# Optimization experiments

Measured on AMD Instinct MI355X. Metric: run time of the kernel, lower is better.

The kernel has to match this reference:

```python
import jax, jax.numpy as jnp
import numpy as np

RES = 32  # voxel grid resolution per axis (cfg.MODEL.NEURAL_POINTS.VOXEL_RES)


def upsample_ac(x, s):
    """Bilinear upsample with align_corners=True. x: [B,C,h,w] -> [B,C,h*s,w*s]."""
    if s == 1:
        return x
    B, C, h, w = x.shape
    H, W = h * s, w * s
    ys = jnp.arange(H, dtype=x.dtype) * ((h - 1) / (H - 1))
    xs = jnp.arange(W, dtype=x.dtype) * ((w - 1) / (W - 1))
    y0 = jnp.floor(ys).astype(jnp.int32)
    x0 = jnp.floor(xs).astype(jnp.int32)
    y1 = jnp.minimum(y0 + 1, h - 1)
    x1 = jnp.minimum(x0 + 1, w - 1)
    wy = (ys - y0.astype(x.dtype))[:, None]  # [H,1]
    wx = (xs - x0.astype(x.dtype))[None, :]  # [1,W]
    top = x[:, :, y0, :]
    bot = x[:, :, y1, :]
    a = top[..., x0]; b = top[..., x1]; c = bot[..., x0]; d = bot[..., x1]
    return (a * (1 - wx) + b * wx) * (1 - wy) + (c * (1 - wx) + d * wx) * wy


def vox_closest(pos):
    """construct_vox_points_closest: per occupied voxel, index of point closest to
    the voxel's point centroid. pos: [N,3] -> [RES^3] int32 indices."""
    N = pos.shape[0]
    Vn = RES ** 3
    mn = pos.min(0)
    mx = pos.max(0)
    vsz = (mx - mn) / RES  # obtain_voxel_size_based_grid_res
    coord = jnp.clip(jnp.floor((pos - mn) / vsz).astype(jnp.int32), 0, RES - 1)
    vid = (coord[:, 0] * RES + coord[:, 1]) * RES + coord[:, 2]  # [N]
    cnt = jax.ops.segment_sum(jnp.ones((N,), pos.dtype), vid, Vn)
    cen = jax.ops.segment_sum(pos, vid, Vn) / jnp.maximum(cnt, 1.0)[:, None]
    d = jnp.sum((pos - cen[vid]) ** 2, axis=-1)  # [N] dist^2 to own-voxel centroid
    dmin = jax.ops.segment_min(d, vid, Vn)
    cand = jnp.where(d <= dmin[vid], jnp.arange(N, dtype=jnp.int32), N)
    midx = jax.ops.segment_min(cand, vid, Vn)
    return jnp.where(midx >= N, 0, midx)  # guard (rare) empty voxels


def reference(rgb, f1, f2, f3, points_pos, points_dir, W1, b1, W2, b2, points_mask):
    V, _, H, W = rgb.shape
    N = V * H * W
    C = 59
    # valid_index = where(points_mask == 1) (mask is all ones -> identity gather)
    valid = jnp.nonzero(points_mask[0] == 1, size=N, fill_value=0)[0]
    pos = points_pos[0, valid]          # [N,3]
    pdir = points_dir[0, valid]         # [N,3]
    # project_point_feats: upsample each pyramid level to full res, concat channels
    ups = [upsample_ac(rgb, 1), upsample_ac(f1, 2), upsample_ac(f2, 4), upsample_ac(f3, 8)]
    pif = jnp.concatenate(ups, axis=1)                       # [V,59,H,W]
    pif = jnp.transpose(pif, (0, 2, 3, 1)).reshape(N, C)     # [N,59]
    color = jax.lax.stop_gradient(jnp.transpose(rgb, (0, 2, 3, 1)).reshape(N, 3))
    pif = pif[valid]
    color = color[valid]
    emb = jnp.concatenate([pif, pdir], axis=-1)              # [N,62]
    midx = vox_closest(pos)                                  # [32768]
    sel_emb = emb[midx]
    sel_pos = pos[midx]
    sel_color = color[midx]
    sel_dir = pdir[midx]
    # point_mlp (premlp_init): 62 -> 256 -> 256
    h = jax.nn.relu(sel_emb @ W1 + b1)
    points_embedding = h @ W2 + b2
    return points_embedding, sel_pos, sel_color, sel_dir


def setup_inputs() -> dict:
    key = jax.random.key(0)
    ks = jax.random.split(key, 10)
    V, H, W = 8, 240, 320
    N = V * H * W
    return {
        "rgb": jax.random.uniform(ks[0], (V, 3, H, W), jnp.float32),
        "f1": jax.random.normal(ks[1], (V, 8, H // 2, W // 2), jnp.float32),
        "f2": jax.random.normal(ks[2], (V, 16, H // 4, W // 4), jnp.float32),
        "f3": jax.random.normal(ks[3], (V, 32, H // 8, W // 8), jnp.float32),
        "points_pos": jax.random.uniform(ks[4], (1, N, 3), jnp.float32),
        "points_dir": jax.random.normal(ks[5], (1, N, 3), jnp.float32),
        "W1": jax.random.normal(ks[6], (62, 256), jnp.float32) * 0.05,
        "b1": jnp.zeros((256,), jnp.float32),
        "W2": jax.random.normal(ks[7], (256, 256), jnp.float32) * 0.05,
        "b2": jnp.zeros((256,), jnp.float32),
        "points_mask": jnp.ones((1, N), jnp.int32),
    }
```

## Files before the change

### kernel.cpp

```cpp
#include <hip/hip_runtime.h>
#include <hip/hip_bf16.h>
#include <limits.h>
#include <stddef.h>

#define NPTS   614400
#define RESV   32
#define NVOX   (RESV*RESV*RESV)
#define IMG_H  240
#define IMG_W  320
#define IMG_HW (IMG_H*IMG_W)
#define INF    __builtin_inff()
#define CAP    64
#define CAPP   32
#define SPILLCAP 4096
#define NBKT   128
#define BCAP   6144
#define BOVFCAP 4096

typedef __attribute__((ext_vector_type(8))) short short8;
typedef __attribute__((ext_vector_type(4))) short s16x4;
typedef __attribute__((ext_vector_type(4))) float f32x4;
typedef float f32x4u __attribute__((ext_vector_type(4), aligned(4)));

__device__ __forceinline__ float fadd_(float a, float b){
#pragma clang fp contract(off)
  return a + b;
}
__device__ __forceinline__ float fsub_(float a, float b){
#pragma clang fp contract(off)
  return a - b;
}
__device__ __forceinline__ float fmul_(float a, float b){
#pragma clang fp contract(off)
  return a * b;
}
__device__ __forceinline__ float fdiv_(float a, float b){
#pragma clang fp contract(off)
  return a / b;
}

__device__ __forceinline__ short f2bf(float x){
  __hip_bfloat16 h = __float2bfloat16(x);
  return *reinterpret_cast<short*>(&h);
}

__global__ void k_prep(int* __restrict__ cnt, int* __restrict__ spillcnt,
                       int* __restrict__ gbase,
                       const float* __restrict__ W1, const float* __restrict__ W2,
                       short* __restrict__ W1t, short* __restrict__ W2t,
                       const float* __restrict__ pos,
                       f32x4* __restrict__ pmin, f32x4* __restrict__ pmax,
                       const float* __restrict__ f1, const float* __restrict__ f2,
                       const float* __restrict__ f3,
                       float* __restrict__ f1t, float* __restrict__ f2t,
                       float* __restrict__ f3t, int tposed){
  int gid = blockIdx.x*blockDim.x + threadIdx.x;
  int stride = gridDim.x*blockDim.x;
  if (gid < NVOX) cnt[gid] = 0;
  if (gid == 0){ spillcnt[0] = 0; spillcnt[1] = 0; }
  if (gid < NBKT) gbase[gid] = 0;
  if (gid < 256*64){
    int n = gid >> 6, k = gid & 63;
    W1t[gid] = (k < 62) ? f2bf(W1[k*256 + n]) : (short)0;
  } else if (gid < 256*64 + 256*256){
    int j = gid - 256*64;
    int n = j >> 8, k = j & 255;
    W2t[j] = f2bf(W2[k*256 + n]);
  }

  if (tposed){
    for (int p = gid; p < 8*19200; p += stride){
      int img = p / 19200, pix = p - img*19200;
      const float* s = f1 + (size_t)img*8*19200 + pix;
      float r[8];
      #pragma unroll
      for (int c = 0; c < 8; c++) r[c] = s[(size_t)c*19200];
      float* d = f1t + (size_t)p*8;
      *(f32x4*)&d[0] = (f32x4){r[0],r[1],r[2],r[3]};
      *(f32x4*)&d[4] = (f32x4){r[4],r[5],r[6],r[7]};
    }
    for (int p = gid; p < 8*4800; p += stride){
      int img = p / 4800, pix = p - img*4800;
      const float* s = f2 + (size_t)img*16*4800 + pix;
      float* d = f2t + (size_t)p*16;
      #pragma unroll
      for (int cq = 0; cq < 4; cq++){
        f32x4 v = { s[(size_t)(4*cq+0)*4800], s[(size_t)(4*cq+1)*4800],
                    s[(size_t)(4*cq+2)*4800], s[(size_t)(4*cq+3)*4800] };
        *(f32x4*)&d[4*cq] = v;
      }
    }
    for (int p = gid; p < 8*1200; p += stride){
      int img = p / 1200, pix = p - img*1200;
      const float* s = f3 + (size_t)img*32*1200 + pix;
      float* d = f3t + (size_t)p*32;
      #pragma unroll
      for (int cq = 0; cq < 8; cq++){
        f32x4 v = { s[(size_t)(4*cq+0)*1200], s[(size_t)(4*cq+1)*1200],
                    s[(size_t)(4*cq+2)*1200], s[(size_t)(4*cq+3)*1200] };
        *(f32x4*)&d[4*cq] = v;
      }
    }
  }

  const f32x4* p4 = (const f32x4*)pos;
  float mn[3] = {  INF,  INF,  INF };
  float mx[3] = { -INF, -INF, -INF };
  for (int t = gid; t < NPTS/4; t += stride){
    f32x4 a = p4[3*t+0], b = p4[3*t+1], c = p4[3*t+2];
    mn[0] = fminf(mn[0], fminf(fminf(a.x, a.w), fminf(b.z, c.y)));
    mx[0] = fmaxf(mx[0], fmaxf(fmaxf(a.x, a.w), fmaxf(b.z, c.y)));
    mn[1] = fminf(mn[1], fminf(fminf(a.y, b.x), fminf(b.w, c.z)));
    mx[1] = fmaxf(mx[1], fmaxf(fmaxf(a.y, b.x), fmaxf(b.w, c.z)));
    mn[2] = fminf(mn[2], fminf(fminf(a.z, b.y), fminf(c.x, c.w)));
    mx[2] = fmaxf(mx[2], fmaxf(fmaxf(a.z, b.y), fmaxf(c.x, c.w)));
  }
  #pragma unroll
  for (int off = 32; off >= 1; off >>= 1){
    #pragma unroll
    for (int c = 0; c < 3; c++){
      mn[c] = fminf(mn[c], __shfl_down(mn[c], off, 64));
      mx[c] = fmaxf(mx[c], __shfl_down(mx[c], off, 64));
    }
  }
  __shared__ float smn[4][3], smx[4][3];
  int lane = threadIdx.x & 63, w = threadIdx.x >> 6;
  if (lane == 0){
    #pragma unroll
    for (int c = 0; c < 3; c++){ smn[w][c] = mn[c]; smx[w][c] = mx[c]; }
  }
  __syncthreads();
  if (threadIdx.x == 0){
    f32x4 a, b;
    a.x = fminf(fminf(smn[0][0], smn[1][0]), fminf(smn[2][0], smn[3][0]));
    a.y = fminf(fminf(smn[0][1], smn[1][1]), fminf(smn[2][1], smn[3][1]));
    a.z = fminf(fminf(smn[0][2], smn[1][2]), fminf(smn[2][2], smn[3][2]));
    a.w = 0.f;
    b.x = fmaxf(fmaxf(smx[0][0], smx[1][0]), fmaxf(smx[2][0], smx[3][0]));
    b.y = fmaxf(fmaxf(smx[0][1], smx[1][1]), fmaxf(smx[2][1], smx[3][1]));
    b.z = fmaxf(fmaxf(smx[0][2], smx[1][2]), fmaxf(smx[2][2], smx[3][2]));
    b.w = 0.f;
    pmin[blockIdx.x] = a;
    pmax[blockIdx.x] = b;
  }
}

__device__ __forceinline__ void reduce_minmax(const f32x4* __restrict__ pmin,
                                              const f32x4* __restrict__ pmax,
                                              float mn[3], float vsz[3]){
  int t = threadIdx.x;
  f32x4 a = pmin[t], b = pmin[t+256];
  f32x4 c = pmax[t], d = pmax[t+256];
  float lmn[3] = { fminf(a.x,b.x), fminf(a.y,b.y), fminf(a.z,b.z) };
  float lmx[3] = { fmaxf(c.x,d.x), fmaxf(c.y,d.y), fmaxf(c.z,d.z) };
  #pragma unroll
  for (int off = 32; off >= 1; off >>= 1){
    #pragma unroll
    for (int k = 0; k < 3; k++){
      lmn[k] = fminf(lmn[k], __shfl_xor(lmn[k], off, 64));
      lmx[k] = fmaxf(lmx[k], __shfl_xor(lmx[k], off, 64));
    }
  }
  __shared__ float smn[4][3], smx[4][3];
  int lane = t & 63, w = t >> 6;
  if (lane == 0){
    #pragma unroll
    for (int k = 0; k < 3; k++){ smn[w][k] = lmn[k]; smx[w][k] = lmx[k]; }
  }
  __syncthreads();
  #pragma unroll
  for (int k = 0; k < 3; k++){
    mn[k] = fminf(fminf(smn[0][k], smn[1][k]), fminf(smn[2][k], smn[3][k]));
    float mx = fmaxf(fmaxf(smx[0][k], smx[1][k]), fmaxf(smx[2][k], smx[3][k]));
    vsz[k] = fdiv_(fsub_(mx, mn[k]), 32.0f);
  }
}

__global__ void k_bucket(const float* __restrict__ pos,
                         const f32x4* __restrict__ pmin, const f32x4* __restrict__ pmax,
                         int* __restrict__ gbase, f32x4* __restrict__ bucketbuf,
                         int* __restrict__ bovfcnt, f32x4* __restrict__ bovf){
  float mn[3], vsz[3];
  reduce_minmax(pmin, pmax, mn, vsz);

  __shared__ int h[NBKT], cur[NBKT];
  int t = threadIdx.x;
  if (t < NBKT) h[t] = 0;
  __syncthreads();

  int base = blockIdx.x*blockDim.x + t;
  const f32x4* p4 = (const f32x4*)pos;
  f32x4 a = p4[3*base+0], b = p4[3*base+1], c = p4[3*base+2];
  float X[4] = {a.x, a.w, b.z, c.y};
  float Y[4] = {a.y, b.x, b.w, c.z};
  float Z[4] = {a.z, b.y, c.x, c.w};
  int vox[4];
  #pragma unroll
  for (int j = 0; j < 4; j++){
    float P[3] = {X[j], Y[j], Z[j]};
    int v = 0;
    #pragma unroll
    for (int k = 0; k < 3; k++){
      float tt = fdiv_(fsub_(P[k], mn[k]), vsz[k]);
      int cc = (int)floorf(tt);
      cc = min(max(cc, 0), RESV-1);
      v = v*RESV + cc;
    }
    vox[j] = v;
    atomicAdd(&h[v >> 8], 1);
  }
  __syncthreads();
  if (t < NBKT) cur[t] = atomicAdd(&gbase[t], h[t]);
  __syncthreads();
  #pragma unroll
  for (int j = 0; j < 4; j++){
    int i = 4*base + j;
    int bk = vox[j] >> 8;
    int r = atomicAdd(&cur[bk], 1);
    f32x4 e = { X[j], Y[j], Z[j], __int_as_float(i) };
    if (r < BCAP){
      bucketbuf[(size_t)bk*BCAP + r] = e;
    } else {
      int so = atomicAdd(bovfcnt, 1);
      if (so < BOVFCAP) bovf[so] = e;
    }
  }
}

__launch_bounds__(512)
__global__ void k_vox2(const f32x4* __restrict__ pmin, const f32x4* __restrict__ pmax,
                       const int* __restrict__ gbase, const f32x4* __restrict__ bucketbuf,
                       const int* __restrict__ bovfcnt, const f32x4* __restrict__ bovf,
                       int* __restrict__ cnt, int* __restrict__ slots,
                       int* __restrict__ spillcnt, int2* __restrict__ spill,
                       f32x4* __restrict__ slotpos, int haspp){
  __shared__ float smn[8][3], smx[8][3];
  __shared__ int cnt_s[256];
  int t = threadIdx.x;
  if (t < 256) cnt_s[t] = 0;

  {
    int tt = t & 255;
    f32x4 a = pmin[tt], b = pmin[tt+256];
    f32x4 c = pmax[tt], d = pmax[tt+256];
    float lmn[3] = { fminf(a.x,b.x), fminf(a.y,b.y), fminf(a.z,b.z) };
    float lmx[3] = { fmaxf(c.x,d.x), fmaxf(c.y,d.y), fmaxf(c.z,d.z) };
    #pragma unroll
    for (int off = 32; off >= 1; off >>= 1){
      #pragma unroll
      for (int k = 0; k < 3; k++){
        lmn[k] = fminf(lmn[k], __shfl_xor(lmn[k], off, 64));
        lmx[k] = fmaxf(lmx[k], __shfl_xor(lmx[k], off, 64));
      }
    }
    int lane = t & 63, w = t >> 6;
    if (lane == 0){
      #pragma unroll
      for (int k = 0; k < 3; k++){ smn[w][k] = lmn[k]; smx[w][k] = lmx[k]; }
    }
  }
  __syncthreads();
  float mn[3], vsz[3];
  #pragma unroll
  for (int k = 0; k < 3; k++){
    float lo = smn[0][k], hi = smx[0][k];
    #pragma unroll
    for (int w = 1; w < 8; w++){ lo = fminf(lo, smn[w][k]); hi = fmaxf(hi, smx[w][k]); }
    mn[k] = lo;
    vsz[k] = fdiv_(fsub_(hi, lo), 32.0f);
  }

  int b = blockIdx.x;
  int nb = min(gbase[b], BCAP);
  for (int j = t; j < nb; j += 512){
    f32x4 rec = bucketbuf[(size_t)b*BCAP + j];
    float P[3] = {rec.x, rec.y, rec.z};
    int v = 0;
    #pragma unroll
    for (int k = 0; k < 3; k++){
      float tt = fdiv_(fsub_(P[k], mn[k]), vsz[k]);
      int cc = (int)floorf(tt);
      cc = min(max(cc, 0), RESV-1);
      v = v*RESV + cc;
    }
    int p = atomicAdd(&cnt_s[v & 255], 1);
    if (haspp && p < CAPP){
      slotpos[(size_t)v*CAPP + p] = rec;
    } else if (p < CAP){
      slots[v*CAP + p] = __float_as_int(rec.w);
    } else {
      int sp = atomicAdd(spillcnt, 1);
      if (sp < SPILLCAP){ int2 e; e.x = v; e.y = __float_as_int(rec.w); spill[sp] = e; }
    }
  }
  int bc = min(*bovfcnt, BOVFCAP);
  for (int j = t; j < bc; j += 512){
    f32x4 rec = bovf[j];
    float P[3] = {rec.x, rec.y, rec.z};
    int v = 0;
    #pragma unroll
    for (int k = 0; k < 3; k++){
      float tt = fdiv_(fsub_(P[k], mn[k]), vsz[k]);
      int cc = (int)floorf(tt);
      cc = min(max(cc, 0), RESV-1);
      v = v*RESV + cc;
    }
    if ((v >> 8) == b){
      int p = atomicAdd(&cnt_s[v & 255], 1);
      if (haspp && p < CAPP){
        slotpos[(size_t)v*CAPP + p] = rec;
      } else if (p < CAP){
        slots[v*CAP + p] = __float_as_int(rec.w);
      } else {
        int sp = atomicAdd(spillcnt, 1);
        if (sp < SPILLCAP){ int2 e; e.x = v; e.y = __float_as_int(rec.w); spill[sp] = e; }
      }
    }
  }
  __syncthreads();
  if (t < 256) cnt[(b << 8) + t] = cnt_s[t];
}

__launch_bounds__(256)
__global__ void k_voxfull(const int* __restrict__ cnt, const int* __restrict__ slots,
                          const int* __restrict__ spillcnt, const int2* __restrict__ spill,
                          const f32x4* __restrict__ slotpos, int haspp,
                          const float* __restrict__ pos,
                          const float* __restrict__ pdir, const float* __restrict__ rgb,
                          const float* __restrict__ f1, const float* __restrict__ f2,
                          const float* __restrict__ f3,
                          const float* __restrict__ f1t, const float* __restrict__ f2t,
                          const float* __restrict__ f3t, int tposed,
                          float* __restrict__ selpos, float* __restrict__ selcol,
                          float* __restrict__ seldir, short* __restrict__ emb){
  __shared__ __align__(16) int skey[4][64];
  __shared__ f32x4 sposl[4][64];
  int lane = threadIdx.x & 63;
  int wv   = threadIdx.x >> 6;
  int v = blockIdx.x*4 + wv;

  f32x4 q = {0.f, 0.f, 0.f, 0.f};
  if (haspp) q = slotpos[(size_t)v*CAPP + (lane & (CAPP-1))];
  int n = cnt[v];

  int m = 0;
  unsigned long long ball = 0;
  float px = 0.f, py = 0.f, pz = 0.f;

  if (n > CAP){
    if (lane == 0){
      int sc = min(*spillcnt, SPILLCAP);
      float sx = 0.f, sy = 0.f, sz = 0.f; int last = -1;
      for (int i = 0; i < n; i++){
        int best = INT_MAX;
        for (int j = 0; j < CAP; j++){
          int id = (haspp && j < CAPP) ? __float_as_int(slotpos[(size_t)v*CAPP + j].w)
                                       : slots[v*CAP + j];
          if (id > last && id < best) best = id;
        }
        for (int j = 0; j < sc; j++){
          int2 e = spill[j];
          if (e.x == v && e.y > last && e.y < best) best = e.y;
        }
        sx = fadd_(sx, pos[3*best+0]);
        sy = fadd_(sy, pos[3*best+1]);
        sz = fadd_(sz, pos[3*best+2]);
        last = best;
      }
      float cf = (float)n;
      float cx = fdiv_(sx, cf), cy = fdiv_(sy, cf), cz = fdiv_(sz, cf);
      float dmin = INF; int mm = 0;
      for (int j = 0; j < CAP + sc; j++){
        int id; int ok = 1;
        if (j < CAP){
          id = (haspp && j < CAPP) ? __float_as_int(slotpos[(size_t)v*CAPP + j].w)
                                   : slots[v*CAP + j];
        } else { int2 e = spill[j-CAP]; ok = (e.x == v); id = e.y; }
        if (!ok) continue;
        float dx = fsub_(pos[3*id+0], cx);
        float dy = fsub_(pos[3*id+1], cy);
        float dz = fsub_(pos[3*id+2], cz);
        float d  = fadd_(fadd_(fmul_(dx,dx), fmul_(dy,dy)), fmul_(dz,dz));
        if (d < dmin || (d == dmin && id < mm)){ dmin = d; mm = id; }
      }
      m = mm;
    }
    m = __shfl(m, 0, 64);
  } else {
    int key = INT_MAX;
    if (haspp && n <= CAPP){
      if (lane < n){
        px = q.x; py = q.y; pz = q.z;
        key = __float_as_int(q.w);
      }
    } else if (haspp){
      if (lane < CAPP){
        px = q.x; py = q.y; pz = q.z;
        key = __float_as_int(q.w);
      } else if (lane < n){
        key = slots[v*CAP + lane];
        if (key < NPTS-1){
          f32x4u qq = *(const f32x4u*)&pos[3*key];
          px = qq.x; py = qq.y; pz = qq.z;
        } else {
          px = pos[3*key+0]; py = pos[3*key+1]; pz = pos[3*key+2];
        }
      }
    } else {
      if (lane < n){
        key = slots[v*CAP + lane];
        if (key < NPTS-1){
          f32x4u qq = *(const f32x4u*)&pos[3*key];
          px = qq.x; py = qq.y; pz = qq.z;
        } else {
          px = pos[3*key+0]; py = pos[3*key+1]; pz = pos[3*key+2];
        }
      }
    }

    skey[wv][lane] = key;
    __builtin_amdgcn_wave_barrier();
    int r = 0;
    {
      int nq = (n + 3) >> 2;
      const int4* k4 = (const int4*)&skey[wv][0];
      for (int j = 0; j < nq; j++){
        int4 kk = k4[j];
        r += (kk.x < key) + (kk.y < key) + (kk.z < key) + (kk.w < key);
      }
    }
    if (lane < n){
      f32x4 e = { px, py, pz, 0.f };
      sposl[wv][r] = e;
    }
    __builtin_amdgcn_wave_barrier();

    float sx = 0.f, sy = 0.f, sz = 0.f;
    for (int i = 0; i < n; i++){
      f32x4 pp = sposl[wv][i];
      sx = fadd_(sx, pp.x);
      sy = fadd_(sy, pp.y);
      sz = fadd_(sz, pp.z);
    }
    float cf = fmaxf((float)n, 1.0f);
    float cx = fdiv_(sx, cf), cy = fdiv_(sy, cf), cz = fdiv_(sz, cf);

    float bd = INF; int bi = 0;
    if (lane < n){
      float dx = fsub_(px, cx), dy = fsub_(py, cy), dz = fsub_(pz, cz);
      bd = fadd_(fadd_(fmul_(dx,dx), fmul_(dy,dy)), fmul_(dz,dz));
      bi = key;
    }
    #pragma unroll
    for (int off = 32; off >= 1; off >>= 1){
      float od = __shfl_xor(bd, off, 64);
      int   oi = __shfl_xor(bi, off, 64);
      if (od < bd || (od == bd && oi < bi)){ bd = od; bi = oi; }
    }
    m = bi;
    ball = __ballot(lane < n && key == m);
  }

  float wx_ = 0.f, wy_ = 0.f, wz_ = 0.f;
  if (ball){
    int wl = (int)(__ffsll((long long)ball) - 1);
    wx_ = __shfl(px, wl, 64);
    wy_ = __shfl(py, wl, 64);
    wz_ = __shfl(pz, wl, 64);
  }

  int img = m / IMG_HW;
  int rem = m - img*IMG_HW;
  int y = rem / IMG_W;
  int x = rem - y*IMG_W;
  int ch = lane;
  float val;
  if (ch < 3){
    val = rgb[((img*3 + ch)*IMG_H + y)*IMG_W + x];
    selcol[3*v+ch] = val;
    float sp = ball ? ((ch == 0) ? wx_ : (ch == 1) ? wy_ : wz_) : pos[3*m+ch];
    selpos[3*v+ch] = sp;
  } else if (ch < 59){
    int lvl = (ch >= 27) ? 2 : ((ch >= 11) ? 1 : 0);
    int c   = ch - ((lvl == 0) ? 3 : ((lvl == 1) ? 11 : 27));
    int C   = 8 << lvl;
    int h   = 120 >> lvl, w = 160 >> lvl;
    float ry = (lvl == 0) ? (119.0f/239.0f) : ((lvl == 1) ? (59.0f/239.0f) : (29.0f/239.0f));
    float rx = (lvl == 0) ? (159.0f/319.0f) : ((lvl == 1) ? (79.0f/319.0f) : (39.0f/319.0f));
    float ys = (float)y * ry;
    float xs = (float)x * rx;
    int y0 = (int)floorf(ys);
    int x0 = (int)floorf(xs);
    int y1 = min(y0+1, h-1);
    int x1 = min(x0+1, w-1);
    float wy = ys - (float)y0;
    float wx = xs - (float)x0;
    float aa, bb, cc, dd;
    if (tposed){
      const float* ft = (lvl == 0) ? f1t : ((lvl == 1) ? f2t : f3t);
      const float* base = ft + (size_t)(img*h*w)*C + c;
      aa = base[(y0*w + x0)*C];
      bb = base[(y0*w + x1)*C];
      cc = base[(y1*w + x0)*C];
      dd = base[(y1*w + x1)*C];
    } else {
      const float* f = (lvl == 0) ? f1 : ((lvl == 1) ? f2 : f3);
      const float* plane = f + ((size_t)img*C + c)*(size_t)(h*w);
      aa = plane[y0*w + x0];
      bb = plane[y0*w + x1];
      cc = plane[y1*w + x0];
      dd = plane[y1*w + x1];
    }
    val = (aa*(1.f-wx) + bb*wx)*(1.f-wy) + (cc*(1.f-wx) + dd*wx)*wy;
  } else if (ch < 62){
    val = pdir[3*m + (ch-59)];
    seldir[3*v+(ch-59)] = val;
  } else {
    val = 0.f;
  }
  emb[(size_t)v*64 + ch] = f2bf(val);
}

#define MLP_BLOCKS 512
#define MLP_TILES  (NVOX/16/MLP_BLOCKS)
__launch_bounds__(256, 2)
__global__ void k_mlp(const short* __restrict__ emb, const short* __restrict__ W1t,
                      const float* __restrict__ b1f, const short* __restrict__ W2t,
                      const float* __restrict__ b2f, float* __restrict__ out){
  __shared__ short Hs[16][264];
  int t    = threadIdx.x;
  int lane = t & 63;
  int wv   = t >> 6;
  int m    = lane & 15;
  int q    = lane >> 4;

  short8 w1f[4][2], w2f[4][8];
  float  b1r[4][4], b2r[4];
  #pragma unroll
  for (int nt = 0; nt < 4; nt++){
    int n = wv*64 + nt*16 + m;
    #pragma unroll
    for (int kq = 0; kq < 2; kq++)
      w1f[nt][kq] = *(const short8*)&W1t[(size_t)n*64 + kq*32 + q*8];
    #pragma unroll
    for (int kq = 0; kq < 8; kq++)
      w2f[nt][kq] = *(const short8*)&W2t[(size_t)n*256 + kq*32 + q*8];
    #pragma unroll
    for (int i = 0; i < 4; i++)
      b1r[nt][i] = b1f[wv*64 + nt*16 + q*4 + i];
    b2r[nt] = b2f[n];
  }

  for (int tt = 0; tt < MLP_TILES; tt++){
    int row0 = (blockIdx.x*MLP_TILES + tt)*16;

    short8 ef0 = *(const short8*)&emb[(size_t)(row0 + m)*64 + q*8];
    short8 ef1 = *(const short8*)&emb[(size_t)(row0 + m)*64 + 32 + q*8];

    #pragma unroll
    for (int nt = 0; nt < 4; nt++){
      f32x4 c = {0.f, 0.f, 0.f, 0.f};
      c = __builtin_amdgcn_mfma_f32_16x16x32_bf16(w1f[nt][0], ef0, c, 0, 0, 0);
      c = __builtin_amdgcn_mfma_f32_16x16x32_bf16(w1f[nt][1], ef1, c, 0, 0, 0);
      s16x4 hv;
      #pragma unroll
      for (int i = 0; i < 4; i++)
        hv[i] = f2bf(fmaxf(c[i] + b1r[nt][i], 0.f));
      *(s16x4*)&Hs[m][wv*64 + nt*16 + q*4] = hv;
    }
    __syncthreads();

    f32x4 acc[4] = {{0,0,0,0},{0,0,0,0},{0,0,0,0},{0,0,0,0}};
    #pragma unroll
    for (int kq = 0; kq < 8; kq++){
      short8 af = *(const short8*)&Hs[m][kq*32 + q*8];
      #pragma unroll
      for (int nt = 0; nt < 4; nt++)
        acc[nt] = __builtin_amdgcn_mfma_f32_16x16x32_bf16(af, w2f[nt][kq], acc[nt], 0, 0, 0);
    }
    __syncthreads();

    #pragma unroll
    for (int nt = 0; nt < 4; nt++){
      int n = wv*64 + nt*16 + m;
      #pragma unroll
      for (int i = 0; i < 4; i++)
        out[(size_t)(row0 + q*4 + i)*256 + n] = acc[nt][i] + b2r[nt];
    }
  }
}

extern "C" void kernel_launch(void* const* d_in, const int* in_sizes, int n_in,
                              void* d_out, int out_size, void* d_ws, size_t ws_size,
                              hipStream_t stream){
  const float* rgb  = (const float*)d_in[0];
  const float* f1   = (const float*)d_in[1];
  const float* f2   = (const float*)d_in[2];
  const float* f3   = (const float*)d_in[3];
  const float* pos  = (const float*)d_in[4];
  const float* pdir = (const float*)d_in[5];
  const float* W1   = (const float*)d_in[6];
  const float* b1   = (const float*)d_in[7];
  const float* W2   = (const float*)d_in[8];
  const float* b2   = (const float*)d_in[9];

  float* out      = (float*)d_out;
  float* out_emb  = out;
  float* out_pos  = out + (size_t)NVOX*256;
  float* out_col  = out_pos + (size_t)NVOX*3;
  float* out_dir  = out_col + (size_t)NVOX*3;

  char* ob = (char*)out_emb;
  f32x4* bucketbuf = (f32x4*)ob;
  f32x4* bovf      = (f32x4*)(ob + (size_t)NBKT*BCAP*16);
  int*   gbase     = (int*)  (ob + (size_t)NBKT*BCAP*16 + (size_t)BOVFCAP*16);

  char* w = (char*)d_ws;
  int*   spillcnt = (int*)w;       w += 64;
  f32x4* pmin     = (f32x4*)w;     w += (size_t)512*16;
  f32x4* pmax     = (f32x4*)w;     w += (size_t)512*16;
  int*   cnt      = (int*)w;       w += (size_t)NVOX*4;
  short* W1t      = (short*)w;     w += (size_t)256*64*2;
  short* W2t      = (short*)w;     w += (size_t)256*256*2;
  short* emb      = (short*)w;     w += (size_t)NVOX*64*2;
  int2*  spill    = (int2*)w;      w += (size_t)SPILLCAP*8;
  int*   slots    = (int*)w;       w += (size_t)NVOX*CAP*4;
  float* f1t      = (float*)w;     w += (size_t)8*19200*8*4;
  float* f2t      = (float*)w;     w += (size_t)8*4800*16*4;
  float* f3t      = (float*)w;     w += (size_t)8*1200*32*4;
  int tposed = ((size_t)(w - (char*)d_ws) <= ws_size) ? 1 : 0;
  f32x4* slotpos  = (f32x4*)w;     w += (size_t)NVOX*CAPP*16;
  int haspp = ((size_t)(w - (char*)d_ws) <= ws_size) ? 1 : 0;

  int* bovfcnt = spillcnt + 1;

  k_prep   <<<512,       256, 0, stream>>>(cnt, spillcnt, gbase, W1, W2, W1t, W2t,
                                           pos, pmin, pmax,
                                           f1, f2, f3, f1t, f2t, f3t, tposed);
  k_bucket <<<NPTS/1024, 256, 0, stream>>>(pos, pmin, pmax, gbase, bucketbuf,
                                           bovfcnt, bovf);
  k_vox2   <<<NBKT,      512, 0, stream>>>(pmin, pmax, gbase, bucketbuf, bovfcnt, bovf,
                                           cnt, slots, spillcnt, spill, slotpos, haspp);
  k_voxfull<<<NVOX/4,    256, 0, stream>>>(cnt, slots, spillcnt, spill, slotpos, haspp,
                                           pos, pdir, rgb, f1, f2, f3,
                                           f1t, f2t, f3t, tposed,
                                           out_pos, out_col, out_dir, emb);
  k_mlp    <<<MLP_BLOCKS,256, 0, stream>>>(emb, W1t, b1, W2t, b2, out_emb);
}
```

Measured before the change: 172.9 us.

## Split voxel-bucket blocks in half and process two voxels per wave

k_vox2 now launches two blocks per bucket, each handling half of the bucket's 256 voxels. The goal is more parallelism across CUs, paid for by each block reading the whole bucket and throwing away half of it. k_voxfull now gives each wavefront two voxels and interleaves their rank, centroid and argmin reductions, to expose more ILP and halve the block count. The catch is higher register use and duplicated gather work per wave.

```diff
diff --git a/kernel.cpp b/kernel.cpp
--- a/kernel.cpp
+++ b/kernel.cpp
@@ -235,9 +235,9 @@
                        int* __restrict__ spillcnt, int2* __restrict__ spill,
                        f32x4* __restrict__ slotpos, int haspp){
   __shared__ float smn[8][3], smx[8][3];
-  __shared__ int cnt_s[256];
+  __shared__ int cnt_s[128];
   int t = threadIdx.x;
-  if (t < 256) cnt_s[t] = 0;
+  if (t < 128) cnt_s[t] = 0;
 
   {
     int tt = t & 255;
@@ -270,7 +270,8 @@
     vsz[k] = fdiv_(fsub_(hi, lo), 32.0f);
   }
 
-  int b = blockIdx.x;
+  int b    = blockIdx.x >> 1;
+  int half = blockIdx.x & 1;
   int nb = min(gbase[b], BCAP);
   for (int j = t; j < nb; j += 512){
     f32x4 rec = bucketbuf[(size_t)b*BCAP + j];
@@ -283,7 +284,8 @@
       cc = min(max(cc, 0), RESV-1);
       v = v*RESV + cc;
     }
-    int p = atomicAdd(&cnt_s[v & 255], 1);
+    if (((v >> 7) & 1) != half) continue;
+    int p = atomicAdd(&cnt_s[v & 127], 1);
     if (haspp && p < CAPP){
       slotpos[(size_t)v*CAPP + p] = rec;
     } else if (p < CAP){
@@ -305,8 +307,8 @@
       cc = min(max(cc, 0), RESV-1);
       v = v*RESV + cc;
     }
-    if ((v >> 8) == b){
-      int p = atomicAdd(&cnt_s[v & 255], 1);
+    if ((v >> 8) == b && ((v >> 7) & 1) == half){
+      int p = atomicAdd(&cnt_s[v & 127], 1);
       if (haspp && p < CAPP){
         slotpos[(size_t)v*CAPP + p] = rec;
       } else if (p < CAP){
@@ -318,7 +320,7 @@
     }
   }
   __syncthreads();
-  if (t < 256) cnt[(b << 8) + t] = cnt_s[t];
+  if (t < 128) cnt[(b << 8) + (half << 7) + t] = cnt_s[t];
 }
 
 __launch_bounds__(256)
@@ -333,192 +335,234 @@
                           const float* __restrict__ f3t, int tposed,
                           float* __restrict__ selpos, float* __restrict__ selcol,
                           float* __restrict__ seldir, short* __restrict__ emb){
-  __shared__ __align__(16) int skey[4][64];
-  __shared__ f32x4 sposl[4][64];
+  __shared__ __align__(16) int skey[8][64];
+  __shared__ f32x4 sposl[8][64];
   int lane = threadIdx.x & 63;
   int wv   = threadIdx.x >> 6;
-  int v = blockIdx.x*4 + wv;
-
-  f32x4 q = {0.f, 0.f, 0.f, 0.f};
-  if (haspp) q = slotpos[(size_t)v*CAPP + (lane & (CAPP-1))];
-  int n = cnt[v];
-
-  int m = 0;
-  unsigned long long ball = 0;
-  float px = 0.f, py = 0.f, pz = 0.f;
-
-  if (n > CAP){
-    if (lane == 0){
-      int sc = min(*spillcnt, SPILLCAP);
-      float sx = 0.f, sy = 0.f, sz = 0.f; int last = -1;
-      for (int i = 0; i < n; i++){
-        int best = INT_MAX;
-        for (int j = 0; j < CAP; j++){
-          int id = (haspp && j < CAPP) ? __float_as_int(slotpos[(size_t)v*CAPP + j].w)
-                                       : slots[v*CAP + j];
-          if (id > last && id < best) best = id;
+  int vb   = blockIdx.x*8 + wv*2;
+
+  f32x4 q[2] = {{0.f,0.f,0.f,0.f},{0.f,0.f,0.f,0.f}};
+  if (haspp){
+    q[0] = slotpos[(size_t)vb*CAPP + (lane & (CAPP-1))];
+    q[1] = slotpos[(size_t)(vb+1)*CAPP + (lane & (CAPP-1))];
+  }
+  int2 nn = *(const int2*)&cnt[vb];
+  int n_[2] = { nn.x, nn.y };
+
+  int   key_[2] = { INT_MAX, INT_MAX };
+  float px_[2] = {0.f,0.f}, py_[2] = {0.f,0.f}, pz_[2] = {0.f,0.f};
+  int   nc_[2], big_[2], mbig_[2] = {0,0};
+
+  #pragma unroll
+  for (int u = 0; u < 2; u++){
+    int v = vb + u, n = n_[u];
+    big_[u] = (n > CAP);
+    nc_[u]  = big_[u] ? 0 : n;
+    if (big_[u]){
+      if (lane == 0){
+        int sc = min(*spillcnt, SPILLCAP);
+        float sx = 0.f, sy = 0.f, sz = 0.f; int last = -1;
+        for (int i = 0; i < n; i++){
+          int best = INT_MAX;
+          for (int j = 0; j < CAP; j++){
+            int id = (haspp && j < CAPP) ? __float_as_int(slotpos[(size_t)v*CAPP + j].w)
+                                         : slots[v*CAP + j];
+            if (id > last && id < best) best = id;
+          }
+          for (int j = 0; j < sc; j++){
+            int2 e = spill[j];
+            if (e.x == v && e.y > last && e.y < best) best = e.y;
+          }
+          sx = fadd_(sx, pos[3*best+0]);
+          sy = fadd_(sy, pos[3*best+1]);
+          sz = fadd_(sz, pos[3*best+2]);
+          last = best;
         }
-        for (int j = 0; j < sc; j++){
-          int2 e = spill[j];
-          if (e.x == v && e.y > last && e.y < best) best = e.y;
+        float cf = (float)n;
+        float cx = fdiv_(sx, cf), cy = fdiv_(sy, cf), cz = fdiv_(sz, cf);
+        float dmin = INF; int mm = 0;
+        for (int j = 0; j < CAP + sc; j++){
+          int id; int ok = 1;
+          if (j < CAP){
+            id = (haspp && j < CAPP) ? __float_as_int(slotpos[(size_t)v*CAPP + j].w)
+                                     : slots[v*CAP + j];
+          } else { int2 e = spill[j-CAP]; ok = (e.x == v); id = e.y; }
+          if (!ok) continue;
+          float dx = fsub_(pos[3*id+0], cx);
+          float dy = fsub_(pos[3*id+1], cy);
+          float dz = fsub_(pos[3*id+2], cz);
+          float d  = fadd_(fadd_(fmul_(dx,dx), fmul_(dy,dy)), fmul_(dz,dz));
+          if (d < dmin || (d == dmin && id < mm)){ dmin = d; mm = id; }
         }
-        sx = fadd_(sx, pos[3*best+0]);
-        sy = fadd_(sy, pos[3*best+1]);
-        sz = fadd_(sz, pos[3*best+2]);
-        last = best;
-      }
-      float cf = (float)n;
-      float cx = fdiv_(sx, cf), cy = fdiv_(sy, cf), cz = fdiv_(sz, cf);
-      float dmin = INF; int mm = 0;
-      for (int j = 0; j < CAP + sc; j++){
-        int id; int ok = 1;
-        if (j < CAP){
-          id = (haspp && j < CAPP) ? __float_as_int(slotpos[(size_t)v*CAPP + j].w)
-                                   : slots[v*CAP + j];
-        } else { int2 e = spill[j-CAP]; ok = (e.x == v); id = e.y; }
-        if (!ok) continue;
-        float dx = fsub_(pos[3*id+0], cx);
-        float dy = fsub_(pos[3*id+1], cy);
-        float dz = fsub_(pos[3*id+2], cz);
-        float d  = fadd_(fadd_(fmul_(dx,dx), fmul_(dy,dy)), fmul_(dz,dz));
-        if (d < dmin || (d == dmin && id < mm)){ dmin = d; mm = id; }
-      }
-      m = mm;
-    }
-    m = __shfl(m, 0, 64);
-  } else {
-    int key = INT_MAX;
-    if (haspp && n <= CAPP){
+        mbig_[u] = mm;
+      }
+      mbig_[u] = __shfl(mbig_[u], 0, 64);
+    } else if (haspp && n <= CAPP){
       if (lane < n){
-        px = q.x; py = q.y; pz = q.z;
-        key = __float_as_int(q.w);
+        px_[u] = q[u].x; py_[u] = q[u].y; pz_[u] = q[u].z;
+        key_[u] = __float_as_int(q[u].w);
       }
     } else if (haspp){
       if (lane < CAPP){
-        px = q.x; py = q.y; pz = q.z;
-        key = __float_as_int(q.w);
+        px_[u] = q[u].x; py_[u] = q[u].y; pz_[u] = q[u].z;
+        key_[u] = __float_as_int(q[u].w);
       } else if (lane < n){
-        key = slots[v*CAP + lane];
+        int key = slots[v*CAP + lane];
         if (key < NPTS-1){
           f32x4u qq = *(const f32x4u*)&pos[3*key];
-          px = qq.x; py = qq.y; pz = qq.z;
+          px_[u] = qq.x; py_[u] = qq.y; pz_[u] = qq.z;
         } else {
-          px = pos[3*key+0]; py = pos[3*key+1]; pz = pos[3*key+2];
+          px_[u] = pos[3*key+0]; py_[u] = pos[3*key+1]; pz_[u] = pos[3*key+2];
         }
+        key_[u] = key;
       }
     } else {
       if (lane < n){
-        key = slots[v*CAP + lane];
+        int key = slots[v*CAP + lane];
         if (key < NPTS-1){
           f32x4u qq = *(const f32x4u*)&pos[3*key];
-          px = qq.x; py = qq.y; pz = qq.z;
+          px_[u] = qq.x; py_[u] = qq.y; pz_[u] = qq.z;
         } else {
-          px = pos[3*key+0]; py = pos[3*key+1]; pz = pos[3*key+2];
+          px_[u] = pos[3*key+0]; py_[u] = pos[3*key+1]; pz_[u] = pos[3*key+2];
         }
-      }
-    }
-
-    skey[wv][lane] = key;
-    __builtin_amdgcn_wave_barrier();
+        key_[u] = key;
+      }
+    }
+  }
+
+  skey[wv*2+0][lane] = key_[0];
+  skey[wv*2+1][lane] = key_[1];
+  __builtin_amdgcn_wave_barrier();
+  int r_[2] = {0,0};
+  #pragma unroll
+  for (int u = 0; u < 2; u++){
+    int key = key_[u];
+    int nq = (nc_[u] + 3) >> 2;
+    const int4* k4 = (const int4*)&skey[wv*2+u][0];
     int r = 0;
-    {
-      int nq = (n + 3) >> 2;
-      const int4* k4 = (const int4*)&skey[wv][0];
-      for (int j = 0; j < nq; j++){
-        int4 kk = k4[j];
-        r += (kk.x < key) + (kk.y < key) + (kk.z < key) + (kk.w < key);
-      }
-    }
-    if (lane < n){
-      f32x4 e = { px, py, pz, 0.f };
-      sposl[wv][r] = e;
-    }
-    __builtin_amdgcn_wave_barrier();
-
-    float sx = 0.f, sy = 0.f, sz = 0.f;
-    for (int i = 0; i < n; i++){
-      f32x4 pp = sposl[wv][i];
-      sx = fadd_(sx, pp.x);
-      sy = fadd_(sy, pp.y);
-      sz = fadd_(sz, pp.z);
-    }
-    float cf = fmaxf((float)n, 1.0f);
-    float cx = fdiv_(sx, cf), cy = fdiv_(sy, cf), cz = fdiv_(sz, cf);
-
-    float bd = INF; int bi = 0;
-    if (lane < n){
-      float dx = fsub_(px, cx), dy = fsub_(py, cy), dz = fsub_(pz, cz);
-      bd = fadd_(fadd_(fmul_(dx,dx), fmul_(dy,dy)), fmul_(dz,dz));
-      bi = key;
-    }
-    #pragma unroll
-    for (int off = 32; off >= 1; off >>= 1){
-      float od = __shfl_xor(bd, off, 64);
-      int   oi = __shfl_xor(bi, off, 64);
-      if (od < bd || (od == bd && oi < bi)){ bd = od; bi = oi; }
-    }
-    m = bi;
-    ball = __ballot(lane < n && key == m);
-  }
-
-  float wx_ = 0.f, wy_ = 0.f, wz_ = 0.f;
-  if (ball){
-    int wl = (int)(__ffsll((long long)ball) - 1);
-    wx_ = __shfl(px, wl, 64);
-    wy_ = __shfl(py, wl, 64);
-    wz_ = __shfl(pz, wl, 64);
-  }
-
-  int img = m / IMG_HW;
-  int rem = m - img*IMG_HW;
-  int y = rem / IMG_W;
-  int x = rem - y*IMG_W;
-  int ch = lane;
-  float val;
-  if (ch < 3){
-    val = rgb[((img*3 + ch)*IMG_H + y)*IMG_W + x];
-    selcol[3*v+ch] = val;
-    float sp = ball ? ((ch == 0) ? wx_ : (ch == 1) ? wy_ : wz_) : pos[3*m+ch];
-    selpos[3*v+ch] = sp;
-  } else if (ch < 59){
-    int lvl = (ch >= 27) ? 2 : ((ch >= 11) ? 1 : 0);
-    int c   = ch - ((lvl == 0) ? 3 : ((lvl == 1) ? 11 : 27));
-    int C   = 8 << lvl;
-    int h   = 120 >> lvl, w = 160 >> lvl;
-    float ry = (lvl == 0) ? (119.0f/239.0f) : ((lvl == 1) ? (59.0f/239.0f) : (29.0f/239.0f));
-    float rx = (lvl == 0) ? (159.0f/319.0f) : ((lvl == 1) ? (79.0f/319.0f) : (39.0f/319.0f));
-    float ys = (float)y * ry;
-    float xs = (float)x * rx;
-    int y0 = (int)floorf(ys);
-    int x0 = (int)floorf(xs);
-    int y1 = min(y0+1, h-1);
-    int x1 = min(x0+1, w-1);
-    float wy = ys - (float)y0;
-    float wx = xs - (float)x0;
-    float aa, bb, cc, dd;
-    if (tposed){
-      const float* ft = (lvl == 0) ? f1t : ((lvl == 1) ? f2t : f3t);
-      const float* base = ft + (size_t)(img*h*w)*C + c;
-      aa = base[(y0*w + x0)*C];
-      bb = base[(y0*w + x1)*C];
-      cc = base[(y1*w + x0)*C];
-      dd = base[(y1*w + x1)*C];
+    for (int j = 0; j < nq; j++){
+      int4 kk = k4[j];
+      r += (kk.x < key) + (kk.y < key) + (kk.z < key) + (kk.w < key);
+    }
+    r_[u] = r;
+  }
+  #pragma unroll
+  for (int u = 0; u < 2; u++){
+    if (lane < nc_[u]){
+      f32x4 e = { px_[u], py_[u], pz_[u], 0.f };
+      sposl[wv*2+u][r_[u]] = e;
+    }
+  }
+  __builtin_amdgcn_wave_barrier();
+
+  float sx0 = 0.f, sy0 = 0.f, sz0 = 0.f;
+  float sx1 = 0.f, sy1 = 0.f, sz1 = 0.f;
+  int nmax = max(nc_[0], nc_[1]);
+  for (int i = 0; i < nmax; i++){
+    if (i < nc_[0]){
+      f32x4 pp = sposl[wv*2+0][i];
+      sx0 = fadd_(sx0, pp.x); sy0 = fadd_(sy0, pp.y); sz0 = fadd_(sz0, pp.z);
+    }
+    if (i < nc_[1]){
+      f32x4 pp = sposl[wv*2+1][i];
+      sx1 = fadd_(sx1, pp.x); sy1 = fadd_(sy1, pp.y); sz1 = fadd_(sz1, pp.z);
+    }
+  }
+  float cf0 = fmaxf((float)nc_[0], 1.0f), cf1 = fmaxf((float)nc_[1], 1.0f);
+  float cx_[2] = { fdiv_(sx0, cf0), fdiv_(sx1, cf1) };
+  float cy_[2] = { fdiv_(sy0, cf0), fdiv_(sy1, cf1) };
+  float cz_[2] = { fdiv_(sz0, cf0), fdiv_(sz1, cf1) };
+
+  float bd0 = INF, bd1 = INF; int bi0 = 0, bi1 = 0;
+  if (lane < nc_[0]){
+    float dx = fsub_(px_[0], cx_[0]), dy = fsub_(py_[0], cy_[0]), dz = fsub_(pz_[0], cz_[0]);
+    bd0 = fadd_(fadd_(fmul_(dx,dx), fmul_(dy,dy)), fmul_(dz,dz));
+    bi0 = key_[0];
+  }
+  if (lane < nc_[1]){
+    float dx = fsub_(px_[1], cx_[1]), dy = fsub_(py_[1], cy_[1]), dz = fsub_(pz_[1], cz_[1]);
+    bd1 = fadd_(fadd_(fmul_(dx,dx), fmul_(dy,dy)), fmul_(dz,dz));
+    bi1 = key_[1];
+  }
+  #pragma unroll
+  for (int off = 32; off >= 1; off >>= 1){
+    float od0 = __shfl_xor(bd0, off, 64); int oi0 = __shfl_xor(bi0, off, 64);
+    float od1 = __shfl_xor(bd1, off, 64); int oi1 = __shfl_xor(bi1, off, 64);
+    if (od0 < bd0 || (od0 == bd0 && oi0 < bi0)){ bd0 = od0; bi0 = oi0; }
+    if (od1 < bd1 || (od1 == bd1 && oi1 < bi1)){ bd1 = od1; bi1 = oi1; }
+  }
+  int m_[2]; unsigned long long ball_[2];
+  m_[0] = big_[0] ? mbig_[0] : bi0;
+  m_[1] = big_[1] ? mbig_[1] : bi1;
+  ball_[0] = big_[0] ? 0ull : __ballot(lane < nc_[0] && key_[0] == bi0);
+  ball_[1] = big_[1] ? 0ull : __ballot(lane < nc_[1] && key_[1] == bi1);
+
+  float wx_[2] = {0.f,0.f}, wy_[2] = {0.f,0.f}, wz_[2] = {0.f,0.f};
+  #pragma unroll
+  for (int u = 0; u < 2; u++){
+    if (ball_[u]){
+      int wl = (int)(__ffsll((long long)ball_[u]) - 1);
+      wx_[u] = __shfl(px_[u], wl, 64);
+      wy_[u] = __shfl(py_[u], wl, 64);
+      wz_[u] = __shfl(pz_[u], wl, 64);
+    }
+  }
+
+  #pragma unroll
+  for (int u = 0; u < 2; u++){
+    int v = vb + u, m = m_[u];
+    int img = m / IMG_HW;
+    int rem = m - img*IMG_HW;
+    int y = rem / IMG_W;
+    int x = rem - y*IMG_W;
+    int ch = lane;
+    float val;
+    if (ch < 3){
+      val = rgb[((img*3 + ch)*IMG_H + y)*IMG_W + x];
+      selcol[3*v+ch] = val;
+      float sp = ball_[u] ? ((ch == 0) ? wx_[u] : (ch == 1) ? wy_[u] : wz_[u])
+                          : pos[3*m+ch];
+      selpos[3*v+ch] = sp;
+    } else if (ch < 59){
+      int lvl = (ch >= 27) ? 2 : ((ch >= 11) ? 1 : 0);
+      int c   = ch - ((lvl == 0) ? 3 : ((lvl == 1) ? 11 : 27));
+      int C   = 8 << lvl;
+      int h   = 120 >> lvl, w = 160 >> lvl;
+      float ry = (lvl == 0) ? (119.0f/239.0f) : ((lvl == 1) ? (59.0f/239.0f) : (29.0f/239.0f));
+      float rx = (lvl == 0) ? (159.0f/319.0f) : ((lvl == 1) ? (79.0f/319.0f) : (39.0f/319.0f));
+      float ys = (float)y * ry;
+      float xs = (float)x * rx;
+      int y0 = (int)floorf(ys);
+      int x0 = (int)floorf(xs);
+      int y1 = min(y0+1, h-1);
+      int x1 = min(x0+1, w-1);
+      float wy = ys - (float)y0;
+      float wx = xs - (float)x0;
+      float aa, bb, cc, dd;
+      if (tposed){
+        const float* ft = (lvl == 0) ? f1t : ((lvl == 1) ? f2t : f3t);
+        const float* base = ft + (size_t)(img*h*w)*C + c;
+        aa = base[(y0*w + x0)*C];
+        bb = base[(y0*w + x1)*C];
+        cc = base[(y1*w + x0)*C];
+        dd = base[(y1*w + x1)*C];
+      } else {
+        const float* f = (lvl == 0) ? f1 : ((lvl == 1) ? f2 : f3);
+        const float* plane = f + ((size_t)img*C + c)*(size_t)(h*w);
+        aa = plane[y0*w + x0];
+        bb = plane[y0*w + x1];
+        cc = plane[y1*w + x0];
+        dd = plane[y1*w + x1];
+      }
+      val = (aa*(1.f-wx) + bb*wx)*(1.f-wy) + (cc*(1.f-wx) + dd*wx)*wy;
+    } else if (ch < 62){
+      val = pdir[3*m + (ch-59)];
+      seldir[3*v+(ch-59)] = val;
     } else {
-      const float* f = (lvl == 0) ? f1 : ((lvl == 1) ? f2 : f3);
-      const float* plane = f + ((size_t)img*C + c)*(size_t)(h*w);
-      aa = plane[y0*w + x0];
-      bb = plane[y0*w + x1];
-      cc = plane[y1*w + x0];
-      dd = plane[y1*w + x1];
-    }
-    val = (aa*(1.f-wx) + bb*wx)*(1.f-wy) + (cc*(1.f-wx) + dd*wx)*wy;
-  } else if (ch < 62){
-    val = pdir[3*m + (ch-59)];
-    seldir[3*v+(ch-59)] = val;
-  } else {
-    val = 0.f;
-  }
-  emb[(size_t)v*64 + ch] = f2bf(val);
+      val = 0.f;
+    }
+    emb[(size_t)v*64 + ch] = f2bf(val);
+  }
 }
 
 #define MLP_BLOCKS 512
@@ -639,9 +683,9 @@
                                            f1, f2, f3, f1t, f2t, f3t, tposed);
   k_bucket <<<NPTS/1024, 256, 0, stream>>>(pos, pmin, pmax, gbase, bucketbuf,
                                            bovfcnt, bovf);
-  k_vox2   <<<NBKT,      512, 0, stream>>>(pmin, pmax, gbase, bucketbuf, bovfcnt, bovf,
+  k_vox2   <<<NBKT*2,    512, 0, stream>>>(pmin, pmax, gbase, bucketbuf, bovfcnt, bovf,
                                            cnt, slots, spillcnt, spill, slotpos, haspp);
-  k_voxfull<<<NVOX/4,    256, 0, stream>>>(cnt, slots, spillcnt, spill, slotpos, haspp,
+  k_voxfull<<<NVOX/8,    256, 0, stream>>>(cnt, slots, spillcnt, spill, slotpos, haspp,
                                            pos, pdir, rgb, f1, f2, f3,
                                            f1t, f2t, f3t, tposed,
                                            out_pos, out_col, out_dir, emb);
```

After: 176.3 us. About the same (+1.9%).
